# Kernel tuning notes

Measured on AMD Instinct MI355X. Metric: run time of the kernel, lower is better.

Reference implementation:

```python
import jax, jax.numpy as jnp
import numpy as np

N_NODES = 100000
N_EDGES = 1200000
N_GRAPHS = 256
D_IN = 8
D_H = 64


def setup_inputs() -> dict:
    key = jax.random.key(0)
    ks = jax.random.split(key, 16)
    x = jax.random.normal(ks[0], (N_NODES, D_IN), dtype=jnp.float32)
    edge_index = jax.random.randint(ks[1], (2, N_EDGES), 0, N_NODES, dtype=jnp.int64)
    batch = jnp.sort(jax.random.randint(ks[2], (N_NODES,), 0, N_GRAPHS, dtype=jnp.int64))

    def lin(k, fan_in, fan_out):
        s = 1.0 / np.sqrt(fan_in)
        return jax.random.uniform(k, (fan_in, fan_out), jnp.float32, -s, s)

    # SAGEConv: lin_l (aggregated neighbors, has bias), lin_r (root, no bias)
    W1l = lin(ks[3], D_IN, D_H); b1 = jnp.zeros((D_H,), jnp.float32); W1r = lin(ks[4], D_IN, D_H)
    W2l = lin(ks[5], D_H, D_H);  b2 = jnp.zeros((D_H,), jnp.float32); W2r = lin(ks[6], D_H, D_H)
    W3l = lin(ks[7], D_H, D_H);  b3 = jnp.zeros((D_H,), jnp.float32); W3r = lin(ks[8], D_H, D_H)
    Wc1 = lin(ks[9], D_H, D_H // 2); bc1 = jnp.zeros((D_H // 2,), jnp.float32)
    Wc2 = lin(ks[10], D_H // 2, 1);  bc2 = jnp.zeros((1,), jnp.float32)
    return dict(x=x, edge_index=edge_index, batch=batch,
                W1l=W1l, b1=b1, W1r=W1r, W2l=W2l, b2=b2, W2r=W2r,
                W3l=W3l, b3=b3, W3r=W3r, Wc1=Wc1, bc1=bc1, Wc2=Wc2, bc2=bc2)


def _sage_conv(x, src, dst, Wl, b, Wr):
    # mean-aggregate messages from source -> target, then two linears
    msg = x[src]                                             # [E, d] gather
    agg = jax.ops.segment_sum(msg, dst, num_segments=N_NODES)
    cnt = jax.ops.segment_sum(jnp.ones((src.shape[0],), x.dtype), dst,
                              num_segments=N_NODES)
    mean = agg / jnp.maximum(cnt, 1.0)[:, None]
    return mean @ Wl + b + x @ Wr


def reference(x, edge_index, batch, W1l, b1, W1r, W2l, b2, W2r,
              W3l, b3, W3r, Wc1, bc1, Wc2, bc2):
    src, dst = edge_index[0], edge_index[1]
    h = jax.nn.relu(_sage_conv(x, src, dst, W1l, b1, W1r))
    h = jax.nn.relu(_sage_conv(h, src, dst, W2l, b2, W2r))
    h = _sage_conv(h, src, dst, W3l, b3, W3r)
    g = jax.ops.segment_sum(h, batch, num_segments=N_GRAPHS)  # global_add_pool
    # dropout is identity in eval mode
    g = jax.nn.relu(g @ Wc1 + bc1)
    return g @ Wc2 + bc2
```

## Files before the change

### kernel.cpp

```cpp
#include <hip/hip_runtime.h>

#define N_NODES 100000
#define N_EDGES 1200000
#define N_GRAPHS 256
#define NBUCK 392
#define EBLK 98
#define EPB 12245
#define DCAP 4608

typedef __attribute__((ext_vector_type(8))) short bf16x8;
typedef __attribute__((ext_vector_type(4))) float f32x4;

__device__ inline unsigned short f2b(float f) {
    union { float f; unsigned u; } c; c.f = f;
    unsigned u = c.u;
    u += 0x7fff + ((u >> 16) & 1);
    return (unsigned short)(u >> 16);
}
__device__ inline float blo(unsigned u) { union { unsigned i; float f; } c; c.i = u << 16; return c.f; }
__device__ inline float bhi(unsigned u) { union { unsigned i; float f; } c; c.i = u & 0xffff0000u; return c.f; }
__device__ inline float b2f(unsigned short h) { union { unsigned i; float f; } c; c.i = ((unsigned)h) << 16; return c.f; }

__global__ __launch_bounds__(256) void setup_kernel(const float* __restrict__ x, unsigned short* __restrict__ xb,
                                                    const float* __restrict__ W2l, const float* __restrict__ W2r,
                                                    unsigned short* __restrict__ pw2, float* __restrict__ zbase,
                                                    const int* __restrict__ ei, int* __restrict__ histm) {
    __shared__ int h[NBUCK];
    int blk = blockIdx.x, tid = threadIdx.x;
    if (blk < 391) {
        int n = blk * 256 + tid;
        if (n < N_NODES) {
            const float4* x4 = (const float4*)x;
            float4 v0 = x4[(size_t)n * 2], v1 = x4[(size_t)n * 2 + 1];
            uint4 p;
            p.x = (unsigned)f2b(v0.x) | ((unsigned)f2b(v0.y) << 16);
            p.y = (unsigned)f2b(v0.z) | ((unsigned)f2b(v0.w) << 16);
            p.z = (unsigned)f2b(v1.x) | ((unsigned)f2b(v1.y) << 16);
            p.w = (unsigned)f2b(v1.z) | ((unsigned)f2b(v1.w) << 16);
            ((uint4*)xb)[n] = p;
        }
    } else if (blk < 423) {
        int r = (blk - 391) * 256 + tid;
        int j = r & 7, lane = (r >> 3) & 63, t = (r >> 9) & 3, s = (r >> 11) & 3;
        int k = s * 32 + (lane >> 4) * 8 + j;
        int n = t * 16 + (lane & 15);
        float v = (k < 64) ? W2l[k * 64 + n] : W2r[(k - 64) * 64 + n];
        pw2[r] = f2b(v);
    } else if (blk < 551) {
        int i = (blk - 423) * 256 + tid;
        zbase[i] = 0.0f;
    } else {
        int k = blk - 551;
        for (int t = tid; t < NBUCK; t += 256) h[t] = 0;
        __syncthreads();
        int e0 = k * EPB, e1 = min(e0 + EPB, N_EDGES);
        for (int e = e0 + tid; e < e1; e += 256) {
            int dd = ei[N_EDGES + e];
            atomicAdd(&h[dd >> 8], 1);
        }
        __syncthreads();
        for (int t = tid; t < NBUCK; t += 256) histm[k * NBUCK + t] = h[t];
    }
}

__global__ __launch_bounds__(512) void bucketB(int* __restrict__ histm, int* __restrict__ bstart) {
    __shared__ int sb[512];
    int tid = threadIdx.x;
    int tot = 0;
    if (tid < NBUCK) {
        for (int k = 0; k < EBLK; k++) tot += histm[k * NBUCK + tid];
    }
    sb[tid] = tot;
    __syncthreads();
    int acc = tot;
    for (int off = 1; off < 512; off <<= 1) {
        int v = (tid >= off) ? sb[tid - off] : 0;
        __syncthreads();
        sb[tid] = acc = acc + v;
        __syncthreads();
    }
    int excl = acc - tot;
    if (tid < NBUCK) {
        bstart[tid] = excl;
        int run = excl;
        for (int k = 0; k < EBLK; k++) {
            int v = histm[k * NBUCK + tid];
            histm[k * NBUCK + tid] = run;
            run += v;
        }
    }
    if (tid == 0) bstart[NBUCK] = N_EDGES;
}

__global__ __launch_bounds__(256) void bucketC(const int* __restrict__ ei, const int* __restrict__ histm,
                                               int* __restrict__ ebuf) {
    __shared__ int cur[NBUCK];
    int k = blockIdx.x, tid = threadIdx.x;
    for (int t = tid; t < NBUCK; t += 256) cur[t] = histm[k * NBUCK + t];
    __syncthreads();
    int e0 = k * EPB, e1 = min(e0 + EPB, N_EDGES);
    for (int e = e0 + tid; e < e1; e += 256) {
        int ss = ei[e];
        int dd = ei[N_EDGES + e];
        int pos = atomicAdd(&cur[dd >> 8], 1);
        ebuf[pos] = (ss << 8) | (dd & 255);
    }
}

__global__ __launch_bounds__(256) void bucketD(const int* __restrict__ ebuf, const int* __restrict__ bstart,
                                               int* __restrict__ rowptr, int* __restrict__ esrc) {
    __shared__ int ecache[DCAP];
    __shared__ int stage[DCAP];
    __shared__ int hist[256], off[256];
    int b = blockIdx.x, tid = threadIdx.x;
    int seg0 = bstart[b], seg1 = bstart[b + 1];
    int cnt = seg1 - seg0;
    hist[tid] = 0;
    int lim = min(cnt, DCAP);
    for (int i = tid; i < lim; i += 256) ecache[i] = ebuf[seg0 + i];
    __syncthreads();
    for (int i = tid; i < cnt; i += 256) {
        int p = (i < DCAP) ? ecache[i] : ebuf[seg0 + i];
        atomicAdd(&hist[p & 255], 1);
    }
    __syncthreads();
    int v = hist[tid];
    off[tid] = v;
    __syncthreads();
    int acc = v;
    for (int o = 1; o < 256; o <<= 1) {
        int t = (tid >= o) ? off[tid - o] : 0;
        __syncthreads();
        off[tid] = acc = acc + t;
        __syncthreads();
    }
    int excl = acc - v;
    rowptr[b * 256 + tid] = seg0 + excl;
    off[tid] = excl;
    __syncthreads();
    if (cnt <= DCAP) {
        for (int i = tid; i < cnt; i += 256) {
            int p = ecache[i];
            int pos = atomicAdd(&off[p & 255], 1);
            stage[pos] = (p >> 8) << 7;
        }
        __syncthreads();
        for (int i = tid; i < cnt; i += 256) esrc[seg0 + i] = stage[i];
    } else {
        for (int i = tid; i < cnt; i += 256) {
            int p = (i < DCAP) ? ecache[i] : ebuf[seg0 + i];
            int pos = atomicAdd(&off[p & 255], 1);
            esrc[seg0 + pos] = (p >> 8) << 7;
        }
    }
}

__global__ __launch_bounds__(256) void layer1_fused(const float* __restrict__ x, const unsigned short* __restrict__ xb,
                                                    const int* __restrict__ rowptr, const int* __restrict__ esrc,
                                                    const float* __restrict__ Wl, const float* __restrict__ b,
                                                    const float* __restrict__ Wr, unsigned short* __restrict__ ob) {
    __shared__ float sa[4][8], sx[4][8];
    int tid = threadIdx.x;
    int sub = tid >> 6, lane = tid & 63;
    int grp = lane >> 2, q = lane & 3;
    int n = blockIdx.x * 4 + sub;
    int r0 = __builtin_amdgcn_readfirstlane(rowptr[n]);
    int r1 = __builtin_amdgcn_readfirstlane(rowptr[n + 1]);
    const unsigned* xbu = (const unsigned*)xb;
    float a0 = 0.f, a1 = 0.f;
#pragma unroll
    for (int c = 0; c < 2; c++) {
        int idx = r0 + 16 * c + grp;
        if (idx < r1) {
            unsigned v = xbu[(esrc[idx] >> 5) + q];
            a0 += blo(v); a1 += bhi(v);
        }
    }
    for (int e = r0 + 32; e < r1; e += 16) {
        int idx = e + grp;
        if (idx < r1) {
            unsigned v = xbu[(esrc[idx] >> 5) + q];
            a0 += blo(v); a1 += bhi(v);
        }
    }
#pragma unroll
    for (int m = 4; m <= 32; m <<= 1) {
        a0 += __shfl_xor(a0, m);
        a1 += __shfl_xor(a1, m);
    }
    if (lane < 4) { sa[sub][2 * lane] = a0; sa[sub][2 * lane + 1] = a1; }
    if (lane >= 8 && lane < 16) sx[sub][lane - 8] = x[(size_t)n * 8 + (lane - 8)];
    __syncthreads();
    float invn = 1.0f / fmaxf((float)(r1 - r0), 1.0f);
    float al = 0.f, ar = 0.f;
#pragma unroll
    for (int kk = 0; kk < 8; kk++) {
        al += sa[sub][kk] * Wl[kk * 64 + lane];
        ar += sx[sub][kk] * Wr[kk * 64 + lane];
    }
    ob[(size_t)n * 64 + lane] = f2b(fmaxf(al * invn + b[lane] + ar, 0.0f));
}

__global__ __launch_bounds__(256) void agg_gemm(const unsigned short* __restrict__ hb,
                                                const int* __restrict__ rowptr,
                                                const int* __restrict__ esrc,
                                                const unsigned short* __restrict__ pw,
                                                const float* __restrict__ bias,
                                                unsigned short* __restrict__ outb,
                                                const int* __restrict__ batch, float* __restrict__ B) {
    __shared__ unsigned short smean[16][64];
    __shared__ int sbat16[16];
    int tid = threadIdx.x;
    int sub = tid >> 6, lane = tid & 63;
    int grp = lane >> 3, q = lane & 7;
    int tile = blockIdx.x;
    const uint4* h16 = (const uint4*)hb;
    if (tid < 16) sbat16[tid] = batch[tile * 16 + tid];
    for (int i = 0; i < 4; i++) {
        int n = tile * 16 + sub * 4 + i;
        int r0 = __builtin_amdgcn_readfirstlane(rowptr[n]);
        int r1 = __builtin_amdgcn_readfirstlane(rowptr[n + 1]);
        uint4 v[3];
#pragma unroll
        for (int c = 0; c < 3; c++) {
            uint4 vv; vv.x = 0u; vv.y = 0u; vv.z = 0u; vv.w = 0u;
            int idx = r0 + 8 * c + grp;
            if (idx < r1) vv = h16[(esrc[idx] >> 4) + q];
            v[c] = vv;
        }
        float a[8];
#pragma unroll
        for (int j = 0; j < 8; j++) a[j] = 0.f;
#pragma unroll
        for (int c = 0; c < 3; c++) {
            a[0] += blo(v[c].x); a[1] += bhi(v[c].x);
            a[2] += blo(v[c].y); a[3] += bhi(v[c].y);
            a[4] += blo(v[c].z); a[5] += bhi(v[c].z);
            a[6] += blo(v[c].w); a[7] += bhi(v[c].w);
        }
        for (int e = r0 + 24; e < r1; e += 8) {
            int idx = e + grp;
            if (idx < r1) {
                uint4 vv = h16[(esrc[idx] >> 4) + q];
                a[0] += blo(vv.x); a[1] += bhi(vv.x);
                a[2] += blo(vv.y); a[3] += bhi(vv.y);
                a[4] += blo(vv.z); a[5] += bhi(vv.z);
                a[6] += blo(vv.w); a[7] += bhi(vv.w);
            }
        }
#pragma unroll
        for (int j = 0; j < 8; j++) {
            a[j] += __shfl_xor(a[j], 8);
            a[j] += __shfl_xor(a[j], 16);
            a[j] += __shfl_xor(a[j], 32);
        }
        if (grp == 0) {
            float invn = 1.0f / fmaxf((float)(r1 - r0), 1.0f);
#pragma unroll
            for (int j = 0; j < 8; j++) smean[sub * 4 + i][q * 8 + j] = f2b(a[j] * invn);
        }
    }
    __syncthreads();
    int col = lane & 15, quad = lane >> 4;
    int m = tile * 16 + col;
    union U { uint4 u; bf16x8 b; };
    U a0, a1, a2, a3;
    a0.u = *(const uint4*)&smean[col][quad * 8];
    a1.u = *(const uint4*)&smean[col][32 + quad * 8];
    const uint4* srow = (const uint4*)(hb + (size_t)m * 64);
    a2.u = srow[quad];
    a3.u = srow[4 + quad];
    const uint4* pwv = (const uint4*)pw;
    int t = sub;
    U b0, b1, b2, b3;
    b0.u = pwv[(0 * 4 + t) * 64 + lane];
    b1.u = pwv[(1 * 4 + t) * 64 + lane];
    b2.u = pwv[(2 * 4 + t) * 64 + lane];
    b3.u = pwv[(3 * 4 + t) * 64 + lane];
    f32x4 acc = {0.f, 0.f, 0.f, 0.f};
    acc = __builtin_amdgcn_mfma_f32_16x16x32_bf16(a0.b, b0.b, acc, 0, 0, 0);
    acc = __builtin_amdgcn_mfma_f32_16x16x32_bf16(a1.b, b1.b, acc, 0, 0, 0);
    acc = __builtin_amdgcn_mfma_f32_16x16x32_bf16(a2.b, b2.b, acc, 0, 0, 0);
    acc = __builtin_amdgcn_mfma_f32_16x16x32_bf16(a3.b, b3.b, acc, 0, 0, 0);
    float bi = bias[t * 16 + col];
    float v[4];
#pragma unroll
    for (int i = 0; i < 4; i++) {
        int node = tile * 16 + quad * 4 + i;
        v[i] = fmaxf(acc[i] + bi, 0.0f);
        outb[(size_t)node * 64 + t * 16 + col] = f2b(v[i]);
    }
    int g0 = sbat16[0], g15 = sbat16[15];
    if (g0 == g15) {
        float s = (v[0] + v[1]) + (v[2] + v[3]);
        s += __shfl_xor(s, 16);
        s += __shfl_xor(s, 32);
        if (quad == 0) atomicAdd(&B[g0 * 64 + t * 16 + col], s);
    } else {
        float accp = 0.f; int cur = sbat16[quad * 4];
#pragma unroll
        for (int i = 0; i < 4; i++) {
            int gi = sbat16[quad * 4 + i];
            if (gi != cur) { atomicAdd(&B[cur * 64 + t * 16 + col], accp); cur = gi; accp = 0.f; }
            accp += v[i];
        }
        atomicAdd(&B[cur * 64 + t * 16 + col], accp);
    }
}

__global__ __launch_bounds__(256) void aggpool3(const unsigned short* __restrict__ hb,
                                                const int* __restrict__ rowptr,
                                                const int* __restrict__ esrc,
                                                const int* __restrict__ batch, float* __restrict__ A) {
    __shared__ float sa[4][64];
    __shared__ int sbat[4];
    int tid = threadIdx.x;
    int sub = tid >> 6, lane = tid & 63;
    int grp = lane >> 3, q = lane & 7;
    int n = blockIdx.x * 4 + sub;
    int r0 = __builtin_amdgcn_readfirstlane(rowptr[n]);
    int r1 = __builtin_amdgcn_readfirstlane(rowptr[n + 1]);
    const uint4* h16 = (const uint4*)hb;
    uint4 v[3];
#pragma unroll
    for (int c = 0; c < 3; c++) {
        uint4 vv; vv.x = 0u; vv.y = 0u; vv.z = 0u; vv.w = 0u;
        int idx = r0 + 8 * c + grp;
        if (idx < r1) {
            int off = esrc[idx];
            vv = h16[(off >> 4) + q];
        }
        v[c] = vv;
    }
    float a[8];
#pragma unroll
    for (int j = 0; j < 8; j++) a[j] = 0.f;
#pragma unroll
    for (int c = 0; c < 3; c++) {
        a[0] += blo(v[c].x); a[1] += bhi(v[c].x);
        a[2] += blo(v[c].y); a[3] += bhi(v[c].y);
        a[4] += blo(v[c].z); a[5] += bhi(v[c].z);
        a[6] += blo(v[c].w); a[7] += bhi(v[c].w);
    }
    for (int e = r0 + 24; e < r1; e += 8) {
        int idx = e + grp;
        if (idx < r1) {
            int off = esrc[idx];
            uint4 vv = h16[(off >> 4) + q];
            a[0] += blo(vv.x); a[1] += bhi(vv.x);
            a[2] += blo(vv.y); a[3] += bhi(vv.y);
            a[4] += blo(vv.z); a[5] += bhi(vv.z);
            a[6] += blo(vv.w); a[7] += bhi(vv.w);
        }
    }
#pragma unroll
    for (int j = 0; j < 8; j++) {
        a[j] += __shfl_xor(a[j], 8);
        a[j] += __shfl_xor(a[j], 16);
        a[j] += __shfl_xor(a[j], 32);
    }
    if (lane == 0) sbat[sub] = batch[n];
    if (grp == 0) {
        float invn = 1.0f / fmaxf((float)(r1 - r0), 1.0f);
#pragma unroll
        for (int j = 0; j < 8; j++) sa[sub][q * 8 + j] = a[j] * invn;
    }
    __syncthreads();
    if (sub == 0) {
        int b0 = sbat[0], b3v = sbat[3];
        if (b0 == b3v) {
            float s = sa[0][lane] + sa[1][lane] + sa[2][lane] + sa[3][lane];
            atomicAdd(&A[b0 * 64 + lane], s);
        } else {
            float acc = sa[0][lane]; int cur = b0;
#pragma unroll
            for (int i = 1; i < 4; i++) {
                int bi = sbat[i];
                if (bi != cur) { atomicAdd(&A[cur * 64 + lane], acc); cur = bi; acc = 0.f; }
                acc += sa[i][lane];
            }
            atomicAdd(&A[cur * 64 + lane], acc);
        }
    }
}

__global__ __launch_bounds__(256) void head2_kernel(const float* __restrict__ A, const float* __restrict__ B,
                                                    const int* __restrict__ batch,
                                                    const float* __restrict__ W3l, const float* __restrict__ b3,
                                                    const float* __restrict__ W3r,
                                                    const float* __restrict__ Wc1, const float* __restrict__ bc1,
                                                    const float* __restrict__ Wc2, const float* __restrict__ bc2,
                                                    float* __restrict__ out) {
    __shared__ float sA[4][64], sB[4][64], sh3[4][64];
    __shared__ float scnt[4];
    int tid = threadIdx.x, sub = tid >> 6, lane = tid & 63;
    int gid = blockIdx.x * 4 + sub;
    sA[sub][lane] = A[gid * 64 + lane];
    sB[sub][lane] = B[gid * 64 + lane];
    if (lane == 0) {
        int lo = 0, hi = N_NODES;
        while (lo < hi) { int mid = (lo + hi) >> 1; if (batch[mid] < gid) lo = mid + 1; else hi = mid; }
        int lo2 = lo, hi2 = N_NODES;
        while (lo2 < hi2) { int mid = (lo2 + hi2) >> 1; if (batch[mid] < gid + 1) lo2 = mid + 1; else hi2 = mid; }
        scnt[sub] = (float)(lo2 - lo);
    }
    __syncthreads();
    float cg = scnt[sub];
    float v = cg * b3[lane];
#pragma unroll 8
    for (int k = 0; k < 64; k++) {
        v += sA[sub][k] * W3l[k * 64 + lane] + sB[sub][k] * W3r[k * 64 + lane];
    }
    sh3[sub][lane] = v;
    __syncthreads();
    int j = lane & 31, kh = lane >> 5;
    float a = 0.f;
#pragma unroll
    for (int kk = 0; kk < 32; kk++) {
        int k = kh * 32 + kk;
        a += sh3[sub][k] * Wc1[k * 32 + j];
    }
    a += __shfl_xor(a, 32);
    float contrib = (lane < 32) ? fmaxf(a + bc1[j], 0.0f) * Wc2[j] : 0.0f;
    contrib += __shfl_xor(contrib, 16);
    contrib += __shfl_xor(contrib, 8);
    contrib += __shfl_xor(contrib, 4);
    contrib += __shfl_xor(contrib, 2);
    contrib += __shfl_xor(contrib, 1);
    if (lane == 0) out[gid] = contrib + bc2[0];
}

extern "C" void kernel_launch(void* const* d_in, const int* in_sizes, int n_in,
                              void* d_out, int out_size, void* d_ws, size_t ws_size,
                              hipStream_t stream) {
    const float* x   = (const float*)d_in[0];
    const int*   ei  = (const int*)d_in[1];
    const int*   bat = (const int*)d_in[2];
    const float* W1l = (const float*)d_in[3];
    const float* b1  = (const float*)d_in[4];
    const float* W1r = (const float*)d_in[5];
    const float* W2l = (const float*)d_in[6];
    const float* b2  = (const float*)d_in[7];
    const float* W2r = (const float*)d_in[8];
    const float* W3l = (const float*)d_in[9];
    const float* b3  = (const float*)d_in[10];
    const float* W3r = (const float*)d_in[11];
    const float* Wc1 = (const float*)d_in[12];
    const float* bc1 = (const float*)d_in[13];
    const float* Wc2 = (const float*)d_in[14];
    const float* bc2 = (const float*)d_in[15];

    float* ws = (float*)d_ws;
    int*    rowptr = (int*)(ws);
    int*    esrc   = (int*)(ws + 100352);
    float*  A      = ws + 1300480;
    float*  B      = ws + 1316864;
    unsigned short* pw2 = (unsigned short*)(ws + 1333504);
    unsigned short* xb  = (unsigned short*)(ws + 1337600);
    unsigned short* hb1 = (unsigned short*)(ws + 1737728);
    unsigned short* hb2 = (unsigned short*)(ws + 4937728);
    int*    ebuf   = (int*)(ws + 8137728);
    int*    histm  = (int*)(ws + 9337728);
    int*    bstart = (int*)(ws + 9376144);

    setup_kernel<<<649, 256, 0, stream>>>(x, xb, W2l, W2r, pw2, A, ei, histm);
    bucketB<<<1, 512, 0, stream>>>(histm, bstart);
    bucketC<<<EBLK, 256, 0, stream>>>(ei, histm, ebuf);
    bucketD<<<NBUCK, 256, 0, stream>>>(ebuf, bstart, rowptr, esrc);

    layer1_fused<<<N_NODES / 4, 256, 0, stream>>>(x, xb, rowptr, esrc, W1l, b1, W1r, hb1);
    agg_gemm<<<N_NODES / 16, 256, 0, stream>>>(hb1, rowptr, esrc, pw2, b2, hb2, bat, B);
    aggpool3<<<N_NODES / 4, 256, 0, stream>>>(hb2, rowptr, esrc, bat, A);

    head2_kernel<<<N_GRAPHS / 4, 256, 0, stream>>>(A, B, bat, W3l, b3, W3r, Wc1, bc1, Wc2, bc2,
                                                   (float*)d_out);
}
```

Baseline: 274.2 us.

## Fuse bucket scan into scatter and layer-1 aggregation into CSR build

Merges the single-block prefix-scan kernel into the scatter kernel: each of the 98 blocks now recomputes the column totals and scan plus its own per-block offsets, and runs with 512 threads. The layer-1 SAGE aggregation and projection move into the bucket-sort kernel, so each thread gathers the neighbours of one node straight from the shared-memory staged edge list and then the block computes the 8->64 projection. Two kernel launches and the reread of rowptr/esrc are removed. In exchange, the scan work is repeated in every block, per-thread serial gathers become unbalanced across nodes, and shared-memory use rises.

```diff
diff --git a/kernel.cpp b/kernel.cpp
--- a/kernel.cpp
+++ b/kernel.cpp
@@ -63,12 +63,14 @@
     }
 }
 
-__global__ __launch_bounds__(512) void bucketB(int* __restrict__ histm, int* __restrict__ bstart) {
+__global__ __launch_bounds__(512) void bucketC(const int* __restrict__ ei, const int* __restrict__ histm,
+                                               int* __restrict__ ebuf, int* __restrict__ bstart) {
     __shared__ int sb[512];
-    int tid = threadIdx.x;
+    __shared__ int cur[NBUCK];
+    int k = blockIdx.x, tid = threadIdx.x;
     int tot = 0;
     if (tid < NBUCK) {
-        for (int k = 0; k < EBLK; k++) tot += histm[k * NBUCK + tid];
+        for (int kk = 0; kk < EBLK; kk++) tot += histm[kk * NBUCK + tid];
     }
     sb[tid] = tot;
     __syncthreads();
@@ -81,25 +83,15 @@
     }
     int excl = acc - tot;
     if (tid < NBUCK) {
-        bstart[tid] = excl;
+        if (k == 0) bstart[tid] = excl;
         int run = excl;
-        for (int k = 0; k < EBLK; k++) {
-            int v = histm[k * NBUCK + tid];
-            histm[k * NBUCK + tid] = run;
-            run += v;
-        }
-    }
-    if (tid == 0) bstart[NBUCK] = N_EDGES;
-}
-
-__global__ __launch_bounds__(256) void bucketC(const int* __restrict__ ei, const int* __restrict__ histm,
-                                               int* __restrict__ ebuf) {
-    __shared__ int cur[NBUCK];
-    int k = blockIdx.x, tid = threadIdx.x;
-    for (int t = tid; t < NBUCK; t += 256) cur[t] = histm[k * NBUCK + t];
+        for (int kk = 0; kk < k; kk++) run += histm[kk * NBUCK + tid];
+        cur[tid] = run;
+    }
+    if (k == 0 && tid == 0) bstart[NBUCK] = N_EDGES;
     __syncthreads();
     int e0 = k * EPB, e1 = min(e0 + EPB, N_EDGES);
-    for (int e = e0 + tid; e < e1; e += 256) {
+    for (int e = e0 + tid; e < e1; e += 512) {
         int ss = ei[e];
         int dd = ei[N_EDGES + e];
         int pos = atomicAdd(&cur[dd >> 8], 1);
@@ -107,15 +99,28 @@
     }
 }
 
-__global__ __launch_bounds__(256) void bucketD(const int* __restrict__ ebuf, const int* __restrict__ bstart,
-                                               int* __restrict__ rowptr, int* __restrict__ esrc) {
+__global__ __launch_bounds__(256) void bucketD_l1(const int* __restrict__ ebuf, const int* __restrict__ bstart,
+                                                  int* __restrict__ rowptr, int* __restrict__ esrc,
+                                                  const unsigned short* __restrict__ xb,
+                                                  const float* __restrict__ W1l, const float* __restrict__ b1v,
+                                                  const float* __restrict__ W1r, unsigned short* __restrict__ hb1) {
     __shared__ int ecache[DCAP];
     __shared__ int stage[DCAP];
     __shared__ int hist[256], off[256];
+    __shared__ float smean[256][8];
+    __shared__ unsigned short sxb[2048];
+    __shared__ float w1l[512], w1r[512], sb1[64];
     int b = blockIdx.x, tid = threadIdx.x;
     int seg0 = bstart[b], seg1 = bstart[b + 1];
     int cnt = seg1 - seg0;
     hist[tid] = 0;
+    int gn = b * 256 + tid;
+    {
+        uint4 z; z.x = 0u; z.y = 0u; z.z = 0u; z.w = 0u;
+        ((uint4*)sxb)[tid] = (gn < N_NODES) ? ((const uint4*)xb)[gn] : z;
+    }
+    for (int i = tid; i < 512; i += 256) { w1l[i] = W1l[i]; w1r[i] = W1r[i]; }
+    if (tid < 64) sb1[tid] = b1v[tid];
     int lim = min(cnt, DCAP);
     for (int i = tid; i < lim; i += 256) ecache[i] = ebuf[seg0 + i];
     __syncthreads();
@@ -138,7 +143,8 @@
     rowptr[b * 256 + tid] = seg0 + excl;
     off[tid] = excl;
     __syncthreads();
-    if (cnt <= DCAP) {
+    bool fits = (cnt <= DCAP);
+    if (fits) {
         for (int i = tid; i < cnt; i += 256) {
             int p = ecache[i];
             int pos = atomicAdd(&off[p & 255], 1);
@@ -153,52 +159,38 @@
             esrc[seg0 + pos] = (p >> 8) << 7;
         }
     }
-}
-
-__global__ __launch_bounds__(256) void layer1_fused(const float* __restrict__ x, const unsigned short* __restrict__ xb,
-                                                    const int* __restrict__ rowptr, const int* __restrict__ esrc,
-                                                    const float* __restrict__ Wl, const float* __restrict__ b,
-                                                    const float* __restrict__ Wr, unsigned short* __restrict__ ob) {
-    __shared__ float sa[4][8], sx[4][8];
-    int tid = threadIdx.x;
-    int sub = tid >> 6, lane = tid & 63;
-    int grp = lane >> 2, q = lane & 3;
-    int n = blockIdx.x * 4 + sub;
-    int r0 = __builtin_amdgcn_readfirstlane(rowptr[n]);
-    int r1 = __builtin_amdgcn_readfirstlane(rowptr[n + 1]);
-    const unsigned* xbu = (const unsigned*)xb;
-    float a0 = 0.f, a1 = 0.f;
-#pragma unroll
-    for (int c = 0; c < 2; c++) {
-        int idx = r0 + 16 * c + grp;
-        if (idx < r1) {
-            unsigned v = xbu[(esrc[idx] >> 5) + q];
-            a0 += blo(v); a1 += bhi(v);
-        }
-    }
-    for (int e = r0 + 32; e < r1; e += 16) {
-        int idx = e + grp;
-        if (idx < r1) {
-            unsigned v = xbu[(esrc[idx] >> 5) + q];
-            a0 += blo(v); a1 += bhi(v);
-        }
-    }
-#pragma unroll
-    for (int m = 4; m <= 32; m <<= 1) {
-        a0 += __shfl_xor(a0, m);
-        a1 += __shfl_xor(a1, m);
-    }
-    if (lane < 4) { sa[sub][2 * lane] = a0; sa[sub][2 * lane + 1] = a1; }
-    if (lane >= 8 && lane < 16) sx[sub][lane - 8] = x[(size_t)n * 8 + (lane - 8)];
-    __syncthreads();
-    float invn = 1.0f / fmaxf((float)(r1 - r0), 1.0f);
-    float al = 0.f, ar = 0.f;
-#pragma unroll
-    for (int kk = 0; kk < 8; kk++) {
-        al += sa[sub][kk] * Wl[kk * 64 + lane];
-        ar += sx[sub][kk] * Wr[kk * 64 + lane];
-    }
-    ob[(size_t)n * 64 + lane] = f2b(fmaxf(al * invn + b[lane] + ar, 0.0f));
+    __syncthreads();
+    const uint4* xb16 = (const uint4*)xb;
+    float a0 = 0.f, a1 = 0.f, a2 = 0.f, a3 = 0.f, a4 = 0.f, a5 = 0.f, a6 = 0.f, a7 = 0.f;
+    for (int i = 0; i < v; i++) {
+        int so = fits ? stage[excl + i] : esrc[seg0 + excl + i];
+        uint4 vv = xb16[so >> 7];
+        a0 += blo(vv.x); a1 += bhi(vv.x);
+        a2 += blo(vv.y); a3 += bhi(vv.y);
+        a4 += blo(vv.z); a5 += bhi(vv.z);
+        a6 += blo(vv.w); a7 += bhi(vv.w);
+    }
+    float invn = 1.0f / fmaxf((float)v, 1.0f);
+    smean[tid][0] = a0 * invn; smean[tid][1] = a1 * invn;
+    smean[tid][2] = a2 * invn; smean[tid][3] = a3 * invn;
+    smean[tid][4] = a4 * invn; smean[tid][5] = a5 * invn;
+    smean[tid][6] = a6 * invn; smean[tid][7] = a7 * invn;
+    __syncthreads();
+    int d = tid & 63, nq = tid >> 6;
+#pragma unroll 4
+    for (int p = 0; p < 64; p++) {
+        int ln = p * 4 + nq;
+        int n = b * 256 + ln;
+        if (n < N_NODES) {
+            float al = 0.f, ar = 0.f;
+#pragma unroll
+            for (int k = 0; k < 8; k++) {
+                al += smean[ln][k] * w1l[k * 64 + d];
+                ar += b2f(sxb[ln * 8 + k]) * w1r[k * 64 + d];
+            }
+            hb1[(size_t)n * 64 + d] = f2b(fmaxf(al + sb1[d] + ar, 0.0f));
+        }
+    }
 }
 
 __global__ __launch_bounds__(256) void agg_gemm(const unsigned short* __restrict__ hb,
@@ -464,11 +456,9 @@
     int*    bstart = (int*)(ws + 9376144);
 
     setup_kernel<<<649, 256, 0, stream>>>(x, xb, W2l, W2r, pw2, A, ei, histm);
-    bucketB<<<1, 512, 0, stream>>>(histm, bstart);
-    bucketC<<<EBLK, 256, 0, stream>>>(ei, histm, ebuf);
-    bucketD<<<NBUCK, 256, 0, stream>>>(ebuf, bstart, rowptr, esrc);
-
-    layer1_fused<<<N_NODES / 4, 256, 0, stream>>>(x, xb, rowptr, esrc, W1l, b1, W1r, hb1);
+    bucketC<<<EBLK, 512, 0, stream>>>(ei, histm, ebuf, bstart);
+    bucketD_l1<<<NBUCK, 256, 0, stream>>>(ebuf, bstart, rowptr, esrc, xb, W1l, b1, W1r, hb1);
+
     agg_gemm<<<N_NODES / 16, 256, 0, stream>>>(hb1, rowptr, esrc, pw2, b2, hb2, bat, B);
     aggpool3<<<N_NODES / 4, 256, 0, stream>>>(hb2, rowptr, esrc, bat, A);
 
```

New measurement: 256.6 us. -6.4%, faster.
